# Optimization experiments

Hardware: AMD Instinct MI355X
Metric: run time of the kernel (lower is better)

Reference implementation:

```python
import jax, jax.numpy as jnp
import numpy as np

D_MODEL = 1024
NUM_HEADS = 16


def setup_inputs() -> dict:
    key = jax.random.key(0)
    ks = jax.random.split(key, 5)
    std = float(np.sqrt(2.0 / (D_MODEL + D_MODEL)))
    def w(k):
        # approximate trunc_normal init with clipped normal (init only; math of fwd unaffected)
        v = jax.random.truncated_normal(k, -3.0, 3.0, (D_MODEL, D_MODEL), jnp.float32) * std
        return v
    x = jax.random.normal(ks[0], (4, 2048, D_MODEL), jnp.float32)
    return {
        "x": x,
        "wq": w(ks[1]),
        "wk": w(ks[2]),
        "wv": w(ks[3]),
        "wo": w(ks[4]),
    }


def reference(x, wq, wk, wv, wo):
    b, s, d = x.shape
    h = NUM_HEADS
    dk = d // h
    # Linear: einsum('o i, ... i -> ... o')
    def proj(w):
        y = jnp.einsum('oi,bsi->bso', w, x)
        return y.reshape(b, s, h, dk).transpose(0, 2, 1, 3)  # b h s dk
    Q, K, V = proj(wq), proj(wk), proj(wv)
    scale = 1.0 / jnp.sqrt(jnp.asarray(dk, x.dtype))
    scores = jnp.einsum('bhqd,bhkd->bhqk', Q, K) * scale
    mask = jnp.tril(jnp.ones((s, s), dtype=bool))
    scores = jnp.where(mask, scores, -jnp.inf)
    attn = jax.nn.softmax(scores, axis=-1)
    out = jnp.einsum('bhqk,bhkd->bhqd', attn, V)
    out = out.transpose(0, 2, 1, 3).reshape(b, s, d)
    return jnp.einsum('oi,bsi->bso', wo, out)
```

## Files before the change

### kernel.cpp

```cpp
#include <hip/hip_runtime.h>
#include <hip/hip_bf16.h>


typedef __bf16 bf16x8 __attribute__((ext_vector_type(8)));
typedef __bf16 bf16x4 __attribute__((ext_vector_type(4)));
typedef float  f32x4  __attribute__((ext_vector_type(4)));
typedef float  f32x16 __attribute__((ext_vector_type(16)));
typedef unsigned int u32x4_t __attribute__((ext_vector_type(4)));

#define GLOBAL_AS __attribute__((address_space(1)))
#define LDS_AS    __attribute__((address_space(3)))

__device__ __forceinline__ void gload16(const void* g, void* l) {
    __builtin_amdgcn_global_load_lds((const GLOBAL_AS void*)g, (LDS_AS void*)l, 16, 0, 0);
}

__device__ __forceinline__ unsigned int cvtpk_bf16(float lo, float hi) {
    unsigned int r;
    asm("v_cvt_pk_bf16_f32 %0, %1, %2" : "=v"(r) : "v"(lo), "v"(hi));
    return r;
}

#define WAITVM8 asm volatile("s_waitcnt vmcnt(8)" ::: "memory")
#define WAITVM6 asm volatile("s_waitcnt vmcnt(6)" ::: "memory")
#define WAITVM0 asm volatile("s_waitcnt vmcnt(0)" ::: "memory")
#define SCHEDB  __builtin_amdgcn_sched_barrier(0)

__global__ __launch_bounds__(256) void cast_kernel(
    const float* __restrict__ x, const float* __restrict__ wq,
    const float* __restrict__ wk, const float* __restrict__ wv,
    const float* __restrict__ wo, __bf16* __restrict__ xb, __bf16* __restrict__ wb) {
    int bid = blockIdx.x;
    const float* src; __bf16* dst; int base;
    if (bid < 4096) {
        src = x; dst = xb; base = bid * 2048;
    } else {
        int r = bid - 4096; int wi = r >> 9;
        src = (wi == 0) ? wq : (wi == 1) ? wk : (wi == 2) ? wv : wo;
        dst = wb + wi * 1048576; base = (r & 511) * 2048;
    }
    int idx = base + threadIdx.x * 8;
    float4 a = *(const float4*)(src + idx);
    float4 b = *(const float4*)(src + idx + 4);
    bf16x8 o;
    o[0] = (__bf16)a.x; o[1] = (__bf16)a.y; o[2] = (__bf16)a.z; o[3] = (__bf16)a.w;
    o[4] = (__bf16)b.x; o[5] = (__bf16)b.y; o[6] = (__bf16)b.z; o[7] = (__bf16)b.w;
    *(bf16x8*)(dst + idx) = o;
}

__global__ __launch_bounds__(512, 2) void gemm_qkv_kernel(
    const __bf16* __restrict__ A, const __bf16* __restrict__ W,
    __bf16* __restrict__ Qb, __bf16* __restrict__ Kb, __bf16* __restrict__ Vt,
    float qscale) {
    __shared__ __align__(16) char lds[147456];
    const int t = threadIdx.x;
    const int wid = t >> 6, lane = t & 63;
    const int g = lane >> 4, m = lane & 15;
    const int wm = wid >> 2, wn = wid & 3;
    const int bid = (blockIdx.x & 7) * 96 + (blockIdx.x >> 3);
    const int mt = bid / 12, nt = bid % 12;
    const int m0 = mt * 128, n0 = nt * 256;
    const bool isV = (n0 >= 2048);

    const __bf16* sA[2]; int dA[2];
#pragma unroll
    for (int i = 0; i < 2; ++i) {
        const int ci = i * 512 + t;
        const int row = ci >> 3;
        const int k8 = (ci & 7) ^ (row & 7);
        sA[i] = A + (size_t)(m0 + row) * 1024 + k8 * 8;
        dA[i] = ci * 16;
    }
    const __bf16* sB[4]; int dB[4];
#pragma unroll
    for (int i = 0; i < 4; ++i) {
        const int ci = i * 512 + t;
        const int row = ci >> 3;
        const int k8 = (ci & 7) ^ (row & 7);
        sB[i] = W + (size_t)(n0 + row) * 1024 + k8 * 8;
        dB[i] = ci * 16;
    }
    auto stage = [&](int kt, char* buf) {
        gload16(sA[0] + kt * 64, buf + dA[0]);
        gload16(sA[1] + kt * 64, buf + dA[1]);
        gload16(sB[0] + kt * 64, buf + 16384 + dB[0]);
        gload16(sB[1] + kt * 64, buf + 16384 + dB[1]);
        gload16(sB[2] + kt * 64, buf + 16384 + dB[2]);
        gload16(sB[3] + kt * 64, buf + 16384 + dB[3]);
    };

    const int sw = (m & 7) << 4;
    const int offA = (wm * 64 + m) * 128 + ((g << 4) ^ sw);
    const int offB = (wn * 64 + m) * 128 + ((g << 4) ^ sw);

    stage(0, lds);
    stage(1, lds + 49152);
    WAITVM6;
    SCHEDB;
    __builtin_amdgcn_s_barrier();
    SCHEDB;

    f32x4 acc[4][4] = {};
    for (int kt = 0; kt < 16; ++kt) {
        char* cbuf = lds + (kt % 3) * 49152;
        if (kt < 14) stage(kt + 2, lds + ((kt + 2) % 3) * 49152);
        const char* bA = cbuf;
        const char* bB = cbuf + 16384;
        bf16x8 a0[4], b0[4], a1[4], b1[4];
#pragma unroll
        for (int i = 0; i < 4; ++i) {
            a0[i] = *(const bf16x8*)(bA + (offA + i * 2048));
            b0[i] = *(const bf16x8*)(bB + (offB + i * 2048));
            a1[i] = *(const bf16x8*)(bA + ((offA + i * 2048) ^ 64));
            b1[i] = *(const bf16x8*)(bB + ((offB + i * 2048) ^ 64));
        }
        __builtin_amdgcn_s_setprio(1);
        if (isV) {
#pragma unroll
            for (int mi = 0; mi < 4; ++mi)
#pragma unroll
                for (int ni = 0; ni < 4; ++ni)
                    acc[mi][ni] = __builtin_amdgcn_mfma_f32_16x16x32_bf16(a0[mi], b0[ni], acc[mi][ni], 0, 0, 0);
#pragma unroll
            for (int mi = 0; mi < 4; ++mi)
#pragma unroll
                for (int ni = 0; ni < 4; ++ni)
                    acc[mi][ni] = __builtin_amdgcn_mfma_f32_16x16x32_bf16(a1[mi], b1[ni], acc[mi][ni], 0, 0, 0);
        } else {
#pragma unroll
            for (int mi = 0; mi < 4; ++mi)
#pragma unroll
                for (int ni = 0; ni < 4; ++ni)
                    acc[mi][ni] = __builtin_amdgcn_mfma_f32_16x16x32_bf16(b0[ni], a0[mi], acc[mi][ni], 0, 0, 0);
#pragma unroll
            for (int mi = 0; mi < 4; ++mi)
#pragma unroll
                for (int ni = 0; ni < 4; ++ni)
                    acc[mi][ni] = __builtin_amdgcn_mfma_f32_16x16x32_bf16(b1[ni], a1[mi], acc[mi][ni], 0, 0, 0);
        }
        __builtin_amdgcn_s_setprio(0);
        if (kt < 14) { WAITVM6; }
        else if (kt == 14) { WAITVM0; }
        if (kt < 15) {
            SCHEDB;
            __builtin_amdgcn_s_barrier();
            SCHEDB;
        }
    }

    if (isV) {
        const int bb = m0 >> 11;
        const int sb = (m0 & 2047) + wm * 64 + 4 * g;
        const int hbase = ((n0 - 2048) >> 6) + wn;
#pragma unroll
        for (int mi = 0; mi < 4; ++mi)
#pragma unroll
            for (int ni = 0; ni < 4; ++ni) {
                const int d = ni * 16 + m;
                bf16x4 pk;
                pk[0] = (__bf16)(acc[mi][ni][0]); pk[1] = (__bf16)(acc[mi][ni][1]);
                pk[2] = (__bf16)(acc[mi][ni][2]); pk[3] = (__bf16)(acc[mi][ni][3]);
                *(bf16x4*)(Vt + ((size_t)(bb * 16 + hbase) * 64 + d) * 2048 + sb + mi * 16) = pk;
            }
    } else {
        __bf16* C = (n0 < 1024) ? Qb : Kb;
        const float sc = (n0 < 1024) ? qscale : 1.f;
        const int cb = (n0 & 1023) + wn * 64 + 4 * g;
        const int row = m0 + wm * 64 + m;
#pragma unroll
        for (int mi = 0; mi < 4; ++mi)
#pragma unroll
            for (int ni = 0; ni < 4; ++ni) {
                bf16x4 pk;
                pk[0] = (__bf16)(acc[mi][ni][0] * sc); pk[1] = (__bf16)(acc[mi][ni][1] * sc);
                pk[2] = (__bf16)(acc[mi][ni][2] * sc); pk[3] = (__bf16)(acc[mi][ni][3] * sc);
                *(bf16x4*)(C + (size_t)(row + mi * 16) * 1024 + cb + ni * 16) = pk;
            }
    }
}

__global__ __launch_bounds__(512, 2) void gemm_out_kernel(
    const __bf16* __restrict__ A, const __bf16* __restrict__ W, float* __restrict__ out) {
    __shared__ __align__(16) char lds[147456];
    const int t = threadIdx.x;
    const int wid = t >> 6, lane = t & 63;
    const int g = lane >> 4, m = lane & 15;
    const int wm = wid >> 2, wn = wid & 3;
    const int bid = (blockIdx.x & 7) * 32 + (blockIdx.x >> 3);
    const int mt = bid >> 2, nt = bid & 3;
    const int m0 = mt * 128, n0 = nt * 256;

    const __bf16* sA[2]; int dA[2];
#pragma unroll
    for (int i = 0; i < 2; ++i) {
        const int ci = i * 512 + t;
        const int row = ci >> 3;
        const int k8 = (ci & 7) ^ (row & 7);
        sA[i] = A + (size_t)(m0 + row) * 1024 + k8 * 8;
        dA[i] = ci * 16;
    }
    const __bf16* sB[4]; int dB[4];
#pragma unroll
    for (int i = 0; i < 4; ++i) {
        const int ci = i * 512 + t;
        const int row = ci >> 3;
        const int k8 = (ci & 7) ^ (row & 7);
        sB[i] = W + (size_t)(n0 + row) * 1024 + k8 * 8;
        dB[i] = ci * 16;
    }
    auto stage = [&](int kt, char* buf) {
        gload16(sA[0] + kt * 64, buf + dA[0]);
        gload16(sA[1] + kt * 64, buf + dA[1]);
        gload16(sB[0] + kt * 64, buf + 16384 + dB[0]);
        gload16(sB[1] + kt * 64, buf + 16384 + dB[1]);
        gload16(sB[2] + kt * 64, buf + 16384 + dB[2]);
        gload16(sB[3] + kt * 64, buf + 16384 + dB[3]);
    };

    const int sw = (m & 7) << 4;
    const int offA = (wm * 64 + m) * 128 + ((g << 4) ^ sw);
    const int offB = (wn * 64 + m) * 128 + ((g << 4) ^ sw);

    stage(0, lds);
    stage(1, lds + 49152);
    WAITVM6;
    SCHEDB;
    __builtin_amdgcn_s_barrier();
    SCHEDB;

    f32x4 acc[4][4] = {};
    for (int kt = 0; kt < 16; ++kt) {
        char* cbuf = lds + (kt % 3) * 49152;
        if (kt < 14) stage(kt + 2, lds + ((kt + 2) % 3) * 49152);
        const char* bA = cbuf;
        const char* bB = cbuf + 16384;
        bf16x8 a0[4], b0[4], a1[4], b1[4];
#pragma unroll
        for (int i = 0; i < 4; ++i) {
            a0[i] = *(const bf16x8*)(bA + (offA + i * 2048));
            b0[i] = *(const bf16x8*)(bB + (offB + i * 2048));
            a1[i] = *(const bf16x8*)(bA + ((offA + i * 2048) ^ 64));
            b1[i] = *(const bf16x8*)(bB + ((offB + i * 2048) ^ 64));
        }
        __builtin_amdgcn_s_setprio(1);
#pragma unroll
        for (int mi = 0; mi < 4; ++mi)
#pragma unroll
            for (int ni = 0; ni < 4; ++ni)
                acc[mi][ni] = __builtin_amdgcn_mfma_f32_16x16x32_bf16(b0[ni], a0[mi], acc[mi][ni], 0, 0, 0);
#pragma unroll
        for (int mi = 0; mi < 4; ++mi)
#pragma unroll
            for (int ni = 0; ni < 4; ++ni)
                acc[mi][ni] = __builtin_amdgcn_mfma_f32_16x16x32_bf16(b1[ni], a1[mi], acc[mi][ni], 0, 0, 0);
        __builtin_amdgcn_s_setprio(0);
        if (kt < 14) { WAITVM6; }
        else if (kt == 14) { WAITVM0; }
        if (kt < 15) {
            SCHEDB;
            __builtin_amdgcn_s_barrier();
            SCHEDB;
        }
    }

    const int row = m0 + wm * 64 + m;
    const int col = n0 + wn * 64 + 4 * g;
#pragma unroll
    for (int mi = 0; mi < 4; ++mi)
#pragma unroll
        for (int ni = 0; ni < 4; ++ni)
            *(f32x4*)(out + (size_t)(row + mi * 16) * 1024 + col + ni * 16) = acc[mi][ni];
}

__global__ __launch_bounds__(128) void attn_kernel(
    const __bf16* __restrict__ Qb, const __bf16* __restrict__ Kb,
    const __bf16* __restrict__ Vt, __bf16* __restrict__ Ob) {
    __shared__ __align__(16) char lds[32768];
    const int t = threadIdx.x;
    const int w = t >> 6, lane = t & 63;
    const int l31 = lane & 31, hi = lane >> 5;
    const int qb = (blockIdx.x >> 3) & 15;
    const int bh = (blockIdx.x & 7) | ((blockIdx.x >> 7) << 3);
    const size_t sbase = (size_t)(bh >> 4) * 2048;
    const int hoff = (bh & 15) * 64;

    const char* Kbase = (const char*)Kb + (sbase * 1024 + hoff) * 2;
    const char* Vbase = (const char*)Vt + (size_t)bh * 262144;
    const int srow = lane >> 3;
    const int scol = ((lane & 7) ^ srow) << 4;
    const int sw = (l31 & 7) << 4;
    int colx[4];
#pragma unroll
    for (int i = 0; i < 4; ++i) colx[i] = (32 * i + 16 * hi) ^ sw;

    auto stage = [&](int kv0, char* lK) {
        char* lV = lK + 8192;
#pragma unroll
        for (int i = 0; i < 4; ++i) {
            const int chunk = i * 2 + w;
            const int row = chunk * 8 + srow;
            gload16(Kbase + (size_t)(kv0 + row) * 2048 + scol, lK + chunk * 1024);
            gload16(Vbase + (size_t)row * 4096 + (size_t)kv0 * 2 + scol, lV + chunk * 1024);
        }
    };

    for (int ph = 0; ph < 2; ++ph) {
        const int s = ph ? (31 - qb) : qb;
        const int q0w = s * 64 + w * 32;
        const int nt = s + 1;
        const int q = q0w + l31;

        const __bf16* qrow = Qb + (sbase + q0w + l31) * 1024 + hoff + 8 * hi;
        bf16x8 qf[4];
#pragma unroll
        for (int c = 0; c < 4; ++c) qf[c] = *(const bf16x8*)(qrow + 16 * c);

        f32x16 o0 = {}, o1 = {};
        float mrun = -__builtin_inff(), lrun = 0.f;

        __builtin_amdgcn_s_barrier();
        stage(0, lds);

        for (int tt = 0; tt < nt; ++tt) {
            const int cur = tt & 1;
            char* lcur = lds + cur * 16384;
            __builtin_amdgcn_s_barrier();
            if (tt + 1 < nt) {
                stage((tt + 1) * 64, lds + (cur ^ 1) * 16384);
                WAITVM8;
            } else {
                WAITVM0;
            }
            __builtin_amdgcn_s_barrier();
            __builtin_amdgcn_sched_barrier(0);

            const int kv0 = tt * 64;
            const char* lK = lcur;
            const char* lV = lcur + 8192;

            f32x16 s0 = {}, s1 = {};
            __builtin_amdgcn_s_setprio(1);
#pragma unroll
            for (int c = 0; c < 4; ++c) {
                bf16x8 k0 = *(const bf16x8*)(lK + l31 * 128 + colx[c]);
                bf16x8 k1 = *(const bf16x8*)(lK + (l31 + 32) * 128 + colx[c]);
                s0 = __builtin_amdgcn_mfma_f32_32x32x16_bf16(k0, qf[c], s0, 0, 0, 0);
                s1 = __builtin_amdgcn_mfma_f32_32x32x16_bf16(k1, qf[c], s1, 0, 0, 0);
            }
            __builtin_amdgcn_s_setprio(0);

            float p[32];
#pragma unroll
            for (int r = 0; r < 16; ++r) { p[r] = s0[r]; p[16 + r] = s1[r]; }
            if (tt == nt - 1) {
#pragma unroll
                for (int r = 0; r < 16; ++r) {
                    const int kvl = (r & 3) + 8 * (r >> 2) + 4 * hi;
                    if (kv0 + kvl > q)      p[r]      = -__builtin_inff();
                    if (kv0 + 32 + kvl > q) p[16 + r] = -__builtin_inff();
                }
            }
            float m8[8];
#pragma unroll
            for (int i = 0; i < 8; ++i)
                m8[i] = fmaxf(fmaxf(p[4 * i], p[4 * i + 1]), fmaxf(p[4 * i + 2], p[4 * i + 3]));
            float tmax = fmaxf(fmaxf(fmaxf(m8[0], m8[1]), fmaxf(m8[2], m8[3])),
                               fmaxf(fmaxf(m8[4], m8[5]), fmaxf(m8[6], m8[7])));
            const bool skip = __all(tmax <= mrun + 8.f);
            if (!skip) {
                float tq = fmaxf(tmax, __shfl_xor(tmax, 32));
                float mnew = fmaxf(mrun, tq);
                float al = __builtin_amdgcn_exp2f(mrun - mnew);
                lrun *= al;
#pragma unroll
                for (int r = 0; r < 16; ++r) { o0[r] *= al; o1[r] *= al; }
                mrun = mnew;
            }
#pragma unroll
            for (int r = 0; r < 32; ++r) p[r] = __builtin_amdgcn_exp2f(p[r] - mrun);
            float s8[8];
#pragma unroll
            for (int i = 0; i < 8; ++i)
                s8[i] = (p[4 * i] + p[4 * i + 1]) + (p[4 * i + 2] + p[4 * i + 3]);
            float rsum = ((s8[0] + s8[1]) + (s8[2] + s8[3])) + ((s8[4] + s8[5]) + (s8[6] + s8[7]));
            rsum += __shfl_xor(rsum, 32);
            lrun += rsum;

            __builtin_amdgcn_s_setprio(1);
#pragma unroll
            for (int cc = 0; cc < 4; ++cc) {
                const int pb = cc * 8;
                unsigned int A0 = cvtpk_bf16(p[pb + 0], p[pb + 1]);
                unsigned int A1 = cvtpk_bf16(p[pb + 2], p[pb + 3]);
                unsigned int B0 = cvtpk_bf16(p[pb + 4], p[pb + 5]);
                unsigned int B1 = cvtpk_bf16(p[pb + 6], p[pb + 7]);
                asm("v_permlane32_swap_b32 %0, %1" : "+v"(A0), "+v"(B0));
                asm("v_permlane32_swap_b32 %0, %1" : "+v"(A1), "+v"(B1));
                u32x4_t wvv; wvv[0] = A0; wvv[1] = A1; wvv[2] = B0; wvv[3] = B1;
                bf16x8 pa = __builtin_bit_cast(bf16x8, wvv);
                const int vcol = (32 * cc + 16 * hi) ^ sw;
                bf16x8 v0 = *(const bf16x8*)(lV + l31 * 128 + vcol);
                bf16x8 v1 = *(const bf16x8*)(lV + (l31 + 32) * 128 + vcol);
                o0 = __builtin_amdgcn_mfma_f32_32x32x16_bf16(v0, pa, o0, 0, 0, 0);
                o1 = __builtin_amdgcn_mfma_f32_32x32x16_bf16(v1, pa, o1, 0, 0, 0);
            }
            __builtin_amdgcn_s_setprio(0);
        }

        const float inv = 1.f / lrun;
        __bf16* orow = Ob + (sbase + q0w + l31) * 1024 + hoff;
#pragma unroll
        for (int rq = 0; rq < 4; ++rq) {
            bf16x4 e0, e1;
#pragma unroll
            for (int j = 0; j < 4; ++j) {
                e0[j] = (__bf16)(o0[rq * 4 + j] * inv);
                e1[j] = (__bf16)(o1[rq * 4 + j] * inv);
            }
            *(bf16x4*)(orow + 4 * hi + 8 * rq) = e0;
            *(bf16x4*)(orow + 32 + 4 * hi + 8 * rq) = e1;
        }
    }
}

extern "C" void kernel_launch(void* const* d_in, const int* in_sizes, int n_in,
                              void* d_out, int out_size, void* d_ws, size_t ws_size,
                              hipStream_t stream) {
    const float* x  = (const float*)d_in[0];
    const float* wq = (const float*)d_in[1];
    const float* wk = (const float*)d_in[2];
    const float* wv = (const float*)d_in[3];
    const float* wo = (const float*)d_in[4];

    char* ws = (char*)d_ws;
    __bf16* xb = (__bf16*)(ws);
    __bf16* wb = (__bf16*)(ws + 16777216);
    __bf16* Qb = (__bf16*)(ws + 25165824);
    __bf16* Kb = (__bf16*)(ws + 41943040);
    __bf16* Vt = (__bf16*)(ws + 58720256);
    __bf16* Ob = (__bf16*)(ws + 75497472);

    const float qscale = 0.18033688011112043f;

    cast_kernel<<<6144, 256, 0, stream>>>(x, wq, wk, wv, wo, xb, wb);
    gemm_qkv_kernel<<<768, 512, 0, stream>>>(xb, wb, Qb, Kb, Vt, qscale);
    attn_kernel<<<1024, 128, 0, stream>>>(Qb, Kb, Vt, Ob);
    gemm_out_kernel<<<256, 512, 0, stream>>>(Ob, wb + 3145728, (float*)d_out);
}
```

Baseline: 188.1 us.

## Restructure attention blocks to 4 waves over 128-row query strips

Each attention block now runs four waves covering a 128-query strip instead of two waves covering paired 64-row strips from opposite ends. K/V tiles staged in LDS are shared by twice as many waves, and each wave issues half the global loads per tile. Load balance across blocks comes from a reversed strip order on alternate block rows rather than the ph loop. The causal mask check moves from the last tile to any tile overlapping the diagonal, since a strip now has two diagonal tiles. The risk is uneven per-block work and more barrier cost with four waves.

```diff
diff --git a/kernel.cpp b/kernel.cpp
--- a/kernel.cpp
+++ b/kernel.cpp
@@ -21,8 +21,8 @@
     return r;
 }
 
-#define WAITVM8 asm volatile("s_waitcnt vmcnt(8)" ::: "memory")
 #define WAITVM6 asm volatile("s_waitcnt vmcnt(6)" ::: "memory")
+#define WAITVM4 asm volatile("s_waitcnt vmcnt(4)" ::: "memory")
 #define WAITVM0 asm volatile("s_waitcnt vmcnt(0)" ::: "memory")
 #define SCHEDB  __builtin_amdgcn_sched_barrier(0)
 
@@ -272,17 +272,24 @@
             *(f32x4*)(out + (size_t)(row + mi * 16) * 1024 + col + ni * 16) = acc[mi][ni];
 }
 
-__global__ __launch_bounds__(128) void attn_kernel(
+__global__ __launch_bounds__(256, 4) void attn_kernel(
     const __bf16* __restrict__ Qb, const __bf16* __restrict__ Kb,
     const __bf16* __restrict__ Vt, __bf16* __restrict__ Ob) {
     __shared__ __align__(16) char lds[32768];
     const int t = threadIdx.x;
     const int w = t >> 6, lane = t & 63;
     const int l31 = lane & 31, hi = lane >> 5;
-    const int qb = (blockIdx.x >> 3) & 15;
-    const int bh = (blockIdx.x & 7) | ((blockIdx.x >> 7) << 3);
+    const int x = blockIdx.x;
+    const int p = x >> 3;
+    const int r = p >> 5, c = p & 31, j = c & 15;
+    const int strip = (r & 1) ? (15 - j) : j;
+    const int bh = (x & 7) | (((c >> 4) + 2 * r) << 3);
     const size_t sbase = (size_t)(bh >> 4) * 2048;
     const int hoff = (bh & 15) * 64;
+
+    const int q0w = strip * 128 + w * 32;
+    const int nt = 2 * (strip + 1);
+    const int q = q0w + l31;
 
     const char* Kbase = (const char*)Kb + (sbase * 1024 + hoff) * 2;
     const char* Vbase = (const char*)Vt + (size_t)bh * 262144;
@@ -296,130 +303,122 @@
     auto stage = [&](int kv0, char* lK) {
         char* lV = lK + 8192;
 #pragma unroll
-        for (int i = 0; i < 4; ++i) {
-            const int chunk = i * 2 + w;
+        for (int i = 0; i < 2; ++i) {
+            const int chunk = i * 4 + w;
             const int row = chunk * 8 + srow;
             gload16(Kbase + (size_t)(kv0 + row) * 2048 + scol, lK + chunk * 1024);
             gload16(Vbase + (size_t)row * 4096 + (size_t)kv0 * 2 + scol, lV + chunk * 1024);
         }
     };
 
-    for (int ph = 0; ph < 2; ++ph) {
-        const int s = ph ? (31 - qb) : qb;
-        const int q0w = s * 64 + w * 32;
-        const int nt = s + 1;
-        const int q = q0w + l31;
-
-        const __bf16* qrow = Qb + (sbase + q0w + l31) * 1024 + hoff + 8 * hi;
-        bf16x8 qf[4];
-#pragma unroll
-        for (int c = 0; c < 4; ++c) qf[c] = *(const bf16x8*)(qrow + 16 * c);
-
-        f32x16 o0 = {}, o1 = {};
-        float mrun = -__builtin_inff(), lrun = 0.f;
-
+    const __bf16* qrow = Qb + (sbase + q0w + l31) * 1024 + hoff + 8 * hi;
+    bf16x8 qf[4];
+#pragma unroll
+    for (int cq = 0; cq < 4; ++cq) qf[cq] = *(const bf16x8*)(qrow + 16 * cq);
+
+    f32x16 o0 = {}, o1 = {};
+    float mrun = -__builtin_inff(), lrun = 0.f;
+
+    stage(0, lds);
+
+    for (int tt = 0; tt < nt; ++tt) {
+        const int cur = tt & 1;
+        char* lcur = lds + cur * 16384;
         __builtin_amdgcn_s_barrier();
-        stage(0, lds);
-
-        for (int tt = 0; tt < nt; ++tt) {
-            const int cur = tt & 1;
-            char* lcur = lds + cur * 16384;
-            __builtin_amdgcn_s_barrier();
-            if (tt + 1 < nt) {
-                stage((tt + 1) * 64, lds + (cur ^ 1) * 16384);
-                WAITVM8;
-            } else {
-                WAITVM0;
+        if (tt + 1 < nt) {
+            stage((tt + 1) * 64, lds + (cur ^ 1) * 16384);
+            WAITVM4;
+        } else {
+            WAITVM0;
+        }
+        __builtin_amdgcn_s_barrier();
+        __builtin_amdgcn_sched_barrier(0);
+
+        const int kv0 = tt * 64;
+        const char* lK = lcur;
+        const char* lV = lcur + 8192;
+
+        f32x16 s0 = {}, s1 = {};
+        __builtin_amdgcn_s_setprio(1);
+#pragma unroll
+        for (int cc = 0; cc < 4; ++cc) {
+            bf16x8 k0 = *(const bf16x8*)(lK + l31 * 128 + colx[cc]);
+            bf16x8 k1 = *(const bf16x8*)(lK + (l31 + 32) * 128 + colx[cc]);
+            s0 = __builtin_amdgcn_mfma_f32_32x32x16_bf16(k0, qf[cc], s0, 0, 0, 0);
+            s1 = __builtin_amdgcn_mfma_f32_32x32x16_bf16(k1, qf[cc], s1, 0, 0, 0);
+        }
+        __builtin_amdgcn_s_setprio(0);
+
+        float pp[32];
+#pragma unroll
+        for (int rr = 0; rr < 16; ++rr) { pp[rr] = s0[rr]; pp[16 + rr] = s1[rr]; }
+        if (kv0 + 63 > q0w) {
+#pragma unroll
+            for (int rr = 0; rr < 16; ++rr) {
+                const int kvl = (rr & 3) + 8 * (rr >> 2) + 4 * hi;
+                if (kv0 + kvl > q)      pp[rr]      = -__builtin_inff();
+                if (kv0 + 32 + kvl > q) pp[16 + rr] = -__builtin_inff();
             }
-            __builtin_amdgcn_s_barrier();
-            __builtin_amdgcn_sched_barrier(0);
-
-            const int kv0 = tt * 64;
-            const char* lK = lcur;
-            const char* lV = lcur + 8192;
-
-            f32x16 s0 = {}, s1 = {};
-            __builtin_amdgcn_s_setprio(1);
-#pragma unroll
-            for (int c = 0; c < 4; ++c) {
-                bf16x8 k0 = *(const bf16x8*)(lK + l31 * 128 + colx[c]);
-                bf16x8 k1 = *(const bf16x8*)(lK + (l31 + 32) * 128 + colx[c]);
-                s0 = __builtin_amdgcn_mfma_f32_32x32x16_bf16(k0, qf[c], s0, 0, 0, 0);
-                s1 = __builtin_amdgcn_mfma_f32_32x32x16_bf16(k1, qf[c], s1, 0, 0, 0);
-            }
-            __builtin_amdgcn_s_setprio(0);
-
-            float p[32];
-#pragma unroll
-            for (int r = 0; r < 16; ++r) { p[r] = s0[r]; p[16 + r] = s1[r]; }
-            if (tt == nt - 1) {
-#pragma unroll
-                for (int r = 0; r < 16; ++r) {
-                    const int kvl = (r & 3) + 8 * (r >> 2) + 4 * hi;
-                    if (kv0 + kvl > q)      p[r]      = -__builtin_inff();
-                    if (kv0 + 32 + kvl > q) p[16 + r] = -__builtin_inff();
-                }
-            }
-            float m8[8];
-#pragma unroll
-            for (int i = 0; i < 8; ++i)
-                m8[i] = fmaxf(fmaxf(p[4 * i], p[4 * i + 1]), fmaxf(p[4 * i + 2], p[4 * i + 3]));
-            float tmax = fmaxf(fmaxf(fmaxf(m8[0], m8[1]), fmaxf(m8[2], m8[3])),
-                               fmaxf(fmaxf(m8[4], m8[5]), fmaxf(m8[6], m8[7])));
-            const bool skip = __all(tmax <= mrun + 8.f);
-            if (!skip) {
-                float tq = fmaxf(tmax, __shfl_xor(tmax, 32));
-                float mnew = fmaxf(mrun, tq);
-                float al = __builtin_amdgcn_exp2f(mrun - mnew);
-                lrun *= al;
-#pragma unroll
-                for (int r = 0; r < 16; ++r) { o0[r] *= al; o1[r] *= al; }
-                mrun = mnew;
-            }
-#pragma unroll
-            for (int r = 0; r < 32; ++r) p[r] = __builtin_amdgcn_exp2f(p[r] - mrun);
-            float s8[8];
-#pragma unroll
-            for (int i = 0; i < 8; ++i)
-                s8[i] = (p[4 * i] + p[4 * i + 1]) + (p[4 * i + 2] + p[4 * i + 3]);
-            float rsum = ((s8[0] + s8[1]) + (s8[2] + s8[3])) + ((s8[4] + s8[5]) + (s8[6] + s8[7]));
-            rsum += __shfl_xor(rsum, 32);
-            lrun += rsum;
-
-            __builtin_amdgcn_s_setprio(1);
-#pragma unroll
-            for (int cc = 0; cc < 4; ++cc) {
-                const int pb = cc * 8;
-                unsigned int A0 = cvtpk_bf16(p[pb + 0], p[pb + 1]);
-                unsigned int A1 = cvtpk_bf16(p[pb + 2], p[pb + 3]);
-                unsigned int B0 = cvtpk_bf16(p[pb + 4], p[pb + 5]);
-                unsigned int B1 = cvtpk_bf16(p[pb + 6], p[pb + 7]);
-                asm("v_permlane32_swap_b32 %0, %1" : "+v"(A0), "+v"(B0));
-                asm("v_permlane32_swap_b32 %0, %1" : "+v"(A1), "+v"(B1));
-                u32x4_t wvv; wvv[0] = A0; wvv[1] = A1; wvv[2] = B0; wvv[3] = B1;
-                bf16x8 pa = __builtin_bit_cast(bf16x8, wvv);
-                const int vcol = (32 * cc + 16 * hi) ^ sw;
-                bf16x8 v0 = *(const bf16x8*)(lV + l31 * 128 + vcol);
-                bf16x8 v1 = *(const bf16x8*)(lV + (l31 + 32) * 128 + vcol);
-                o0 = __builtin_amdgcn_mfma_f32_32x32x16_bf16(v0, pa, o0, 0, 0, 0);
-                o1 = __builtin_amdgcn_mfma_f32_32x32x16_bf16(v1, pa, o1, 0, 0, 0);
-            }
-            __builtin_amdgcn_s_setprio(0);
-        }
-
-        const float inv = 1.f / lrun;
-        __bf16* orow = Ob + (sbase + q0w + l31) * 1024 + hoff;
-#pragma unroll
-        for (int rq = 0; rq < 4; ++rq) {
-            bf16x4 e0, e1;
-#pragma unroll
-            for (int j = 0; j < 4; ++j) {
-                e0[j] = (__bf16)(o0[rq * 4 + j] * inv);
-                e1[j] = (__bf16)(o1[rq * 4 + j] * inv);
-            }
-            *(bf16x4*)(orow + 4 * hi + 8 * rq) = e0;
-            *(bf16x4*)(orow + 32 + 4 * hi + 8 * rq) = e1;
-        }
+        }
+        float m8[8];
+#pragma unroll
+        for (int i = 0; i < 8; ++i)
+            m8[i] = fmaxf(fmaxf(pp[4 * i], pp[4 * i + 1]), fmaxf(pp[4 * i + 2], pp[4 * i + 3]));
+        float tmax = fmaxf(fmaxf(fmaxf(m8[0], m8[1]), fmaxf(m8[2], m8[3])),
+                           fmaxf(fmaxf(m8[4], m8[5]), fmaxf(m8[6], m8[7])));
+        const bool skip = __all(tmax <= mrun + 8.f);
+        if (!skip) {
+            float tq = fmaxf(tmax, __shfl_xor(tmax, 32));
+            float mnew = fmaxf(mrun, tq);
+            float al = __builtin_amdgcn_exp2f(mrun - mnew);
+            lrun *= al;
+#pragma unroll
+            for (int rr = 0; rr < 16; ++rr) { o0[rr] *= al; o1[rr] *= al; }
+            mrun = mnew;
+        }
+#pragma unroll
+        for (int rr = 0; rr < 32; ++rr) pp[rr] = __builtin_amdgcn_exp2f(pp[rr] - mrun);
+        float s8[8];
+#pragma unroll
+        for (int i = 0; i < 8; ++i)
+            s8[i] = (pp[4 * i] + pp[4 * i + 1]) + (pp[4 * i + 2] + pp[4 * i + 3]);
+        float rsum = ((s8[0] + s8[1]) + (s8[2] + s8[3])) + ((s8[4] + s8[5]) + (s8[6] + s8[7]));
+        rsum += __shfl_xor(rsum, 32);
+        lrun += rsum;
+
+        __builtin_amdgcn_s_setprio(1);
+#pragma unroll
+        for (int cc = 0; cc < 4; ++cc) {
+            const int pb = cc * 8;
+            unsigned int A0 = cvtpk_bf16(pp[pb + 0], pp[pb + 1]);
+            unsigned int A1 = cvtpk_bf16(pp[pb + 2], pp[pb + 3]);
+            unsigned int B0 = cvtpk_bf16(pp[pb + 4], pp[pb + 5]);
+            unsigned int B1 = cvtpk_bf16(pp[pb + 6], pp[pb + 7]);
+            asm("v_permlane32_swap_b32 %0, %1" : "+v"(A0), "+v"(B0));
+            asm("v_permlane32_swap_b32 %0, %1" : "+v"(A1), "+v"(B1));
+            u32x4_t wvv; wvv[0] = A0; wvv[1] = A1; wvv[2] = B0; wvv[3] = B1;
+            bf16x8 pa = __builtin_bit_cast(bf16x8, wvv);
+            const int vcol = (32 * cc + 16 * hi) ^ sw;
+            bf16x8 v0 = *(const bf16x8*)(lV + l31 * 128 + vcol);
+            bf16x8 v1 = *(const bf16x8*)(lV + (l31 + 32) * 128 + vcol);
+            o0 = __builtin_amdgcn_mfma_f32_32x32x16_bf16(v0, pa, o0, 0, 0, 0);
+            o1 = __builtin_amdgcn_mfma_f32_32x32x16_bf16(v1, pa, o1, 0, 0, 0);
+        }
+        __builtin_amdgcn_s_setprio(0);
+    }
+
+    const float inv = 1.f / lrun;
+    __bf16* orow = Ob + (sbase + q0w + l31) * 1024 + hoff;
+#pragma unroll
+    for (int rq = 0; rq < 4; ++rq) {
+        bf16x4 e0, e1;
+#pragma unroll
+        for (int jj = 0; jj < 4; ++jj) {
+            e0[jj] = (__bf16)(o0[rq * 4 + jj] * inv);
+            e1[jj] = (__bf16)(o1[rq * 4 + jj] * inv);
+        }
+        *(bf16x4*)(orow + 4 * hi + 8 * rq) = e0;
+        *(bf16x4*)(orow + 32 + 4 * hi + 8 * rq) = e1;
     }
 }
 
@@ -444,6 +443,6 @@
 
     cast_kernel<<<6144, 256, 0, stream>>>(x, wq, wk, wv, wo, xb, wb);
     gemm_qkv_kernel<<<768, 512, 0, stream>>>(xb, wb, Qb, Kb, Vt, qscale);
-    attn_kernel<<<1024, 128, 0, stream>>>(Qb, Kb, Vt, Ob);
+    attn_kernel<<<1024, 256, 0, stream>>>(Qb, Kb, Vt, Ob);
     gemm_out_kernel<<<256, 512, 0, stream>>>(Ob, wb + 3145728, (float*)d_out);
 }
```

After: 205.0 us. +9.0%, slower.
